# Kernel tuning notes

Hardware: AMD Instinct MI355X
Metric: run time of the kernel (lower is better)

Reference implementation:

```python
import jax, jax.numpy as jnp
import numpy as np

B, S, D, H = 2, 2048, 1024, 16
DK = D // H


def setup_inputs() -> dict:
    key = jax.random.key(0)
    ks = jax.random.split(key, 12)
    scale = 1.0 / np.sqrt(D)
    inp = {
        "q": jax.random.normal(ks[0], (B, S, D), jnp.float32),
        "k": jax.random.normal(ks[1], (B, S, D), jnp.float32),
        "v": jax.random.normal(ks[2], (B, S, D), jnp.float32),
        # causal mask: 1 = attend, 0 = mask, broadcastable to (B, 1, S, S)
        "mask": jnp.tril(jnp.ones((S, S), jnp.int32))[None, None, :, :],
        "Wq": jax.random.normal(ks[3], (D, D), jnp.float32) * scale,
        "bq": jax.random.normal(ks[4], (D,), jnp.float32) * scale,
        "Wk": jax.random.normal(ks[5], (D, D), jnp.float32) * scale,
        "bk": jax.random.normal(ks[6], (D,), jnp.float32) * scale,
        "Wv": jax.random.normal(ks[7], (D, D), jnp.float32) * scale,
        "bv": jax.random.normal(ks[8], (D,), jnp.float32) * scale,
        "Wo": jax.random.normal(ks[9], (D, D), jnp.float32) * scale,
        "bo": jax.random.normal(ks[10], (D,), jnp.float32) * scale,
    }
    return inp


def _split_heads(x):
    b, s, _ = x.shape
    return x.reshape(b, s, H, DK).transpose(0, 2, 1, 3)  # (b, h, s, dk)


def reference(q, k, v, mask, Wq, bq, Wk, bk, Wv, bv, Wo, bo):
    Q = _split_heads(q @ Wq.T + bq)
    K = _split_heads(k @ Wk.T + bk)
    V = _split_heads(v @ Wv.T + bv)
    scores = jnp.einsum("bhqd,bhkd->bhqk", Q, K) * (DK ** -0.5)
    scores = jnp.where(mask == 0, -jnp.inf, scores)
    attn = jax.nn.softmax(scores, axis=-1)  # dropout p=0.0 -> identity
    out = jnp.einsum("bhqk,bhkd->bhqd", attn, V)
    out = out.transpose(0, 2, 1, 3).reshape(q.shape[0], q.shape[1], D)
    return out @ Wo.T + bo
```

## Files before the change

### kernel.cpp

```cpp
#include <hip/hip_runtime.h>


#define S_LEN 2048
#define NHEAD 16
#define DMODEL 1024
#define DKH 64
#define LDA 72

typedef unsigned short u16;
typedef __attribute__((ext_vector_type(4))) short short4v;
typedef __attribute__((ext_vector_type(8))) short short8;
typedef __attribute__((ext_vector_type(8))) __bf16 bf16x8;
typedef __attribute__((ext_vector_type(4))) float f32x4;

__device__ inline u16 f2bf(float f) {
  return __builtin_bit_cast(u16, (__bf16)f);
}

__device__ inline f32x4 mfma16x16(bf16x8 a, bf16x8 b, f32x4 c) {
  return __builtin_amdgcn_mfma_f32_16x16x32_bf16(a, b, c, 0, 0, 0);
}

__device__ inline short8 pack8(float4 a, float4 b) {
  short8 r;
  r[0] = (short)f2bf(a.x); r[1] = (short)f2bf(a.y);
  r[2] = (short)f2bf(a.z); r[3] = (short)f2bf(a.w);
  r[4] = (short)f2bf(b.x); r[5] = (short)f2bf(b.y);
  r[6] = (short)f2bf(b.z); r[7] = (short)f2bf(b.w);
  return r;
}

typedef const __attribute__((address_space(1))) unsigned GU32;
typedef __attribute__((address_space(3))) unsigned LU32;
__device__ inline void gl2lds16(const void* g, void* l) {
  __builtin_amdgcn_global_load_lds((GU32*)g, (LU32*)l, 16, 0, 0);
}

#define SWZ(row, col8) (((row) * 8 + ((col8) ^ ((row) & 7))) * 8)

__global__ __launch_bounds__(256)
void conv_bf16(const float* __restrict__ w0, const float* __restrict__ w1,
               const float* __restrict__ w2, const float* __restrict__ w3,
               const float* __restrict__ aq, const float* __restrict__ ak,
               const float* __restrict__ av,
               u16* __restrict__ o0, u16* __restrict__ o1,
               u16* __restrict__ o2, u16* __restrict__ o3,
               u16* __restrict__ oq, u16* __restrict__ ok, u16* __restrict__ ov)
{
  const int y = blockIdx.y;
  const float* s; u16* d; int n;
  switch (y) {
    case 0: s = w0; d = o0; n = 1 << 20; break;
    case 1: s = w1; d = o1; n = 1 << 20; break;
    case 2: s = w2; d = o2; n = 1 << 20; break;
    case 3: s = w3; d = o3; n = 1 << 20; break;
    case 4: s = aq; d = oq; n = 1 << 22; break;
    case 5: s = ak; d = ok; n = 1 << 22; break;
    default: s = av; d = ov; n = 1 << 22; break;
  }
  const int i = (blockIdx.x * 256 + threadIdx.x) * 8;
  if (i >= n) return;
  float4 a = *(const float4*)&s[i];
  float4 b = *(const float4*)&s[i + 4];
  *(short8*)&d[i] = pack8(a, b);
}

__global__ __launch_bounds__(256)
void conv_w(const float* __restrict__ w0, const float* __restrict__ w1,
            const float* __restrict__ w2, const float* __restrict__ w3,
            u16* __restrict__ o0, u16* __restrict__ o1,
            u16* __restrict__ o2, u16* __restrict__ o3)
{
  const int z = blockIdx.y;
  const float* s = z == 0 ? w0 : z == 1 ? w1 : z == 2 ? w2 : w3;
  u16* d = z == 0 ? o0 : z == 1 ? o1 : z == 2 ? o2 : o3;
  const int i = (blockIdx.x * 256 + threadIdx.x) * 8;
  float4 a = *(const float4*)&s[i];
  float4 b = *(const float4*)&s[i + 4];
  *(short8*)&d[i] = pack8(a, b);
}

__global__ __launch_bounds__(256)
void proj_gemm_bf16(const u16* __restrict__ Aqb, const u16* __restrict__ Akb,
                    const u16* __restrict__ Avb,
                    const u16* __restrict__ Bq, const u16* __restrict__ Bk,
                    const u16* __restrict__ Bv,
                    const float* __restrict__ cq, const float* __restrict__ ck,
                    const float* __restrict__ cv,
                    u16* __restrict__ Oq, u16* __restrict__ Ok, u16* __restrict__ Ov)
{
  __shared__ u16 SM[4 * 8192];

  const int hw = blockIdx.x + (blockIdx.y << 3) + (blockIdx.z << 8);
  const int xcd = hw & 7, sq = hw >> 3;
  const int pan = sq % 12, xb = sq / 12;
  const int p = pan * 8 + xcd;
  const int zz = p >> 5, py = p & 31;

  const u16* Ab = zz == 0 ? Aqb : zz == 1 ? Akb : Avb;
  const u16* Wb = zz == 0 ? Bq : zz == 1 ? Bk : Bv;
  const float* bias = zz == 0 ? cq : zz == 1 ? ck : cv;

  const int t = threadIdx.x;
  const int lane = t & 63;
  const int wv = t >> 6;
  const int wm = wv >> 1, wn = wv & 1;
  const int g = lane >> 4, lr = lane & 15;
  const int bm = py << 7, bn = xb << 7;
  const int K = DMODEL;

  auto STAGE = [&](int buf, int kt) {
    const int k0 = kt << 6;
    u16* Asb = SM + buf * 8192;
    u16* Bsb = SM + 16384 + buf * 8192;
#pragma unroll
    for (int i = 0; i < 4; ++i) {
      int c = t + (i << 8);
      int row = c >> 3, col8 = c & 7;
      int c8s = col8 ^ (row & 7);
      gl2lds16(&Ab[(size_t)(bm + row) * K + k0 + c8s * 8], &Asb[c * 8]);
      gl2lds16(&Wb[(size_t)(bn + row) * K + k0 + c8s * 8], &Bsb[c * 8]);
    }
  };

  f32x4 acc[4][4] = {};
  STAGE(0, 0);
  __syncthreads();
  for (int kt = 0; kt < 16; ++kt) {
    const int cur = kt & 1;
    if (kt + 1 < 16) STAGE(cur ^ 1, kt + 1);
    u16* Asb = SM + cur * 8192;
    u16* Bsb = SM + 16384 + cur * 8192;
    bf16x8 af[2][4], bf[2][4];
#pragma unroll
    for (int kc = 0; kc < 2; ++kc)
#pragma unroll
      for (int f = 0; f < 4; ++f) {
        af[kc][f] = *(const bf16x8*)&Asb[SWZ(wm * 64 + f * 16 + lr, kc * 4 + g)];
        bf[kc][f] = *(const bf16x8*)&Bsb[SWZ(wn * 64 + f * 16 + lr, kc * 4 + g)];
      }
#pragma unroll
    for (int kc = 0; kc < 2; ++kc)
#pragma unroll
      for (int fm = 0; fm < 4; ++fm)
#pragma unroll
        for (int fn = 0; fn < 4; ++fn)
          acc[fm][fn] = mfma16x16(af[kc][fm], bf[kc][fn], acc[fm][fn]);
    __syncthreads();
  }

  if (zz == 2) {
    u16* TL = SM;
    const int b = bm >> 11, s0 = bm & (S_LEN - 1), h0 = bn >> 6;
#pragma unroll
    for (int hh = 0; hh < 2; ++hh) {
      __syncthreads();
      if (wn == hh) {
#pragma unroll
        for (int fm = 0; fm < 4; ++fm)
#pragma unroll
          for (int fn = 0; fn < 4; ++fn) {
            const int lch = fn * 16 + lr;
            const float bb = bias[bn + hh * 64 + lch];
#pragma unroll
            for (int r = 0; r < 4; ++r)
              TL[lch * 132 + wm * 64 + fm * 16 + g * 4 + r] = f2bf(acc[fm][fn][r] + bb);
          }
      }
      __syncthreads();
#pragma unroll
      for (int i = 0; i < 4; ++i) {
        int c = t + (i << 8);
        int dk = c >> 4, sc = (c & 15) << 3;
        short8 vv = *(const short8*)&TL[dk * 132 + sc];
        *(short8*)&Ov[(((size_t)(b * NHEAD + h0 + hh)) * DKH + dk) * S_LEN + s0 + sc] = vv;
      }
    }
  } else {
    u16* Out = zz == 0 ? Oq : Ok;
#pragma unroll
    for (int fm = 0; fm < 4; ++fm)
#pragma unroll
      for (int fn = 0; fn < 4; ++fn) {
        const int col = bn + wn * 64 + fn * 16 + lr;
        const int h = col >> 6, dk = col & (DKH - 1);
        const float bb = bias[col];
#pragma unroll
        for (int r = 0; r < 4; ++r) {
          const int row = bm + wm * 64 + fm * 16 + g * 4 + r;
          const int b = row >> 11, s = row & (S_LEN - 1);
          Out[(((size_t)(b * NHEAD + h)) * S_LEN + s) * DKH + dk] = f2bf(acc[fm][fn][r] + bb);
        }
      }
  }
}

__global__ __launch_bounds__(256)
void proj_gemm_f32(const float* __restrict__ Aq, const float* __restrict__ Akk,
                   const float* __restrict__ Av,
                   const u16* __restrict__ Bq, const u16* __restrict__ Bk,
                   const u16* __restrict__ Bv,
                   const float* __restrict__ cq, const float* __restrict__ ck,
                   const float* __restrict__ cv,
                   u16* __restrict__ Oq, u16* __restrict__ Ok, u16* __restrict__ Ov)
{
  __shared__ u16 SM[3 * 8192];
  u16* As = SM;
  u16* Bs0 = SM + 8192;
  u16* Bs1 = SM + 16384;

  const int hw = blockIdx.x + (blockIdx.y << 3) + (blockIdx.z << 8);
  const int xcd = hw & 7, sq = hw >> 3;
  const int pan = sq % 12, xb = sq / 12;
  const int p = pan * 8 + xcd;
  const int zz = p >> 5, py = p & 31;

  const float* Af = zz == 0 ? Aq : zz == 1 ? Akk : Av;
  const u16* Wb = zz == 0 ? Bq : zz == 1 ? Bk : Bv;
  const float* bias = zz == 0 ? cq : zz == 1 ? ck : cv;

  const int t = threadIdx.x;
  const int lane = t & 63;
  const int wv = t >> 6;
  const int wm = wv >> 1, wn = wv & 1;
  const int g = lane >> 4, lr = lane & 15;
  const int bm = py << 7, bn = xb << 7;
  const int K = DMODEL;

  float4 ax[4], ay[4];
  auto ALOAD = [&](int kt) {
    const int k0 = kt << 6;
#pragma unroll
    for (int i = 0; i < 4; ++i) {
      int c = t + (i << 8);
      int row = c >> 3, col8 = c & 7;
      const float* src = &Af[(size_t)(bm + row) * K + k0 + col8 * 8];
      ax[i] = *(const float4*)src;
      ay[i] = *(const float4*)(src + 4);
    }
  };
  auto AWRITE = [&]() {
#pragma unroll
    for (int i = 0; i < 4; ++i) {
      int c = t + (i << 8);
      int row = c >> 3, col8 = c & 7;
      *(short8*)&As[SWZ(row, col8)] = pack8(ax[i], ay[i]);
    }
  };
  auto BSTAGE = [&](u16* buf, int kt) {
    const int k0 = kt << 6;
#pragma unroll
    for (int i = 0; i < 4; ++i) {
      int c = t + (i << 8);
      int row = c >> 3, col8 = c & 7;
      int c8s = col8 ^ (row & 7);
      gl2lds16(&Wb[(size_t)(bn + row) * K + k0 + c8s * 8], &buf[c * 8]);
    }
  };

  f32x4 acc[4][4] = {};
  ALOAD(0);
  BSTAGE(Bs0, 0);
  AWRITE();
  __syncthreads();
  for (int kt = 0; kt < 16; ++kt) {
    u16* Bcur = (kt & 1) ? Bs1 : Bs0;
    u16* Bnxt = (kt & 1) ? Bs0 : Bs1;
    const bool more = (kt + 1 < 16);
    if (more) { ALOAD(kt + 1); BSTAGE(Bnxt, kt + 1); }
    bf16x8 af[2][4], bf[2][4];
#pragma unroll
    for (int kc = 0; kc < 2; ++kc)
#pragma unroll
      for (int f = 0; f < 4; ++f) {
        af[kc][f] = *(const bf16x8*)&As[SWZ(wm * 64 + f * 16 + lr, kc * 4 + g)];
        bf[kc][f] = *(const bf16x8*)&Bcur[SWZ(wn * 64 + f * 16 + lr, kc * 4 + g)];
      }
#pragma unroll
    for (int kc = 0; kc < 2; ++kc)
#pragma unroll
      for (int fm = 0; fm < 4; ++fm)
#pragma unroll
        for (int fn = 0; fn < 4; ++fn)
          acc[fm][fn] = mfma16x16(af[kc][fm], bf[kc][fn], acc[fm][fn]);
    __syncthreads();
    if (more) {
      AWRITE();
      __syncthreads();
    }
  }

  if (zz == 2) {
    u16* TL = SM;
    const int b = bm >> 11, s0 = bm & (S_LEN - 1), h0 = bn >> 6;
#pragma unroll
    for (int hh = 0; hh < 2; ++hh) {
      __syncthreads();
      if (wn == hh) {
#pragma unroll
        for (int fm = 0; fm < 4; ++fm)
#pragma unroll
          for (int fn = 0; fn < 4; ++fn) {
            const int lch = fn * 16 + lr;
            const float bb = bias[bn + hh * 64 + lch];
#pragma unroll
            for (int r = 0; r < 4; ++r)
              TL[lch * 132 + wm * 64 + fm * 16 + g * 4 + r] = f2bf(acc[fm][fn][r] + bb);
          }
      }
      __syncthreads();
#pragma unroll
      for (int i = 0; i < 4; ++i) {
        int c = t + (i << 8);
        int dk = c >> 4, sc = (c & 15) << 3;
        short8 vv = *(const short8*)&TL[dk * 132 + sc];
        *(short8*)&Ov[(((size_t)(b * NHEAD + h0 + hh)) * DKH + dk) * S_LEN + s0 + sc] = vv;
      }
    }
  } else {
    u16* Out = zz == 0 ? Oq : Ok;
#pragma unroll
    for (int fm = 0; fm < 4; ++fm)
#pragma unroll
      for (int fn = 0; fn < 4; ++fn) {
        const int col = bn + wn * 64 + fn * 16 + lr;
        const int h = col >> 6, dk = col & (DKH - 1);
        const float bb = bias[col];
#pragma unroll
        for (int r = 0; r < 4; ++r) {
          const int row = bm + wm * 64 + fm * 16 + g * 4 + r;
          const int b = row >> 11, s = row & (S_LEN - 1);
          Out[(((size_t)(b * NHEAD + h)) * S_LEN + s) * DKH + dk] = f2bf(acc[fm][fn][r] + bb);
        }
      }
  }
}

__global__ __launch_bounds__(256)
void out_gemm(const u16* __restrict__ Ao, const u16* __restrict__ Wb,
              const float* __restrict__ bias, float* __restrict__ Out)
{
  __shared__ u16 SM[4 * 8192];
  const int hw = blockIdx.x + (blockIdx.y << 3);
  const int xcd = hw & 7, sq = hw >> 3;
  const int pan = sq & 3, xb = sq >> 2;
  const int prow = pan * 8 + xcd;

  const int t = threadIdx.x;
  const int lane = t & 63;
  const int wv = t >> 6;
  const int wm = wv >> 1, wn = wv & 1;
  const int g = lane >> 4, lr = lane & 15;
  const int bm = prow << 7, bn = xb << 7;
  const int K = DMODEL;

  auto STAGE = [&](int buf, int kt) {
    const int k0 = kt << 6;
    u16* Asb = SM + buf * 8192;
    u16* Bsb = SM + 16384 + buf * 8192;
#pragma unroll
    for (int i = 0; i < 4; ++i) {
      int c = t + (i << 8);
      int row = c >> 3, col8 = c & 7;
      int c8s = col8 ^ (row & 7);
      int grow = bm + row;
      int b = grow >> 11, s = grow & (S_LEN - 1);
      int k = k0 + c8s * 8;
      int h = k >> 6, dk = k & (DKH - 1);
      gl2lds16(&Ao[(((size_t)(b * NHEAD + h)) * S_LEN + s) * DKH + dk], &Asb[c * 8]);
      gl2lds16(&Wb[(size_t)(bn + row) * K + k0 + c8s * 8], &Bsb[c * 8]);
    }
  };

  f32x4 acc[4][4] = {};
  STAGE(0, 0);
  __syncthreads();
  for (int kt = 0; kt < 16; ++kt) {
    const int cur = kt & 1;
    if (kt + 1 < 16) STAGE(cur ^ 1, kt + 1);
    u16* Asb = SM + cur * 8192;
    u16* Bsb = SM + 16384 + cur * 8192;
    bf16x8 af[2][4], bf[2][4];
#pragma unroll
    for (int kc = 0; kc < 2; ++kc)
#pragma unroll
      for (int f = 0; f < 4; ++f) {
        af[kc][f] = *(const bf16x8*)&Asb[SWZ(wm * 64 + f * 16 + lr, kc * 4 + g)];
        bf[kc][f] = *(const bf16x8*)&Bsb[SWZ(wn * 64 + f * 16 + lr, kc * 4 + g)];
      }
#pragma unroll
    for (int kc = 0; kc < 2; ++kc)
#pragma unroll
      for (int fm = 0; fm < 4; ++fm)
#pragma unroll
        for (int fn = 0; fn < 4; ++fn)
          acc[fm][fn] = mfma16x16(af[kc][fm], bf[kc][fn], acc[fm][fn]);
    __syncthreads();
  }
#pragma unroll
  for (int fm = 0; fm < 4; ++fm)
#pragma unroll
    for (int fn = 0; fn < 4; ++fn) {
      const int col = bn + wn * 64 + fn * 16 + lr;
      const float bb = bias[col];
#pragma unroll
      for (int r = 0; r < 4; ++r) {
        const int row = bm + wm * 64 + fm * 16 + g * 4 + r;
        Out[(size_t)row * DMODEL + col] = acc[fm][fn][r] + bb;
      }
    }
}

__global__ __launch_bounds__(256)
void attn_fwd(const u16* __restrict__ Qh, const u16* __restrict__ Kh,
              const u16* __restrict__ Vtg, u16* __restrict__ Ao)
{
  __shared__ u16 Ks[2][64 * LDA];
  __shared__ u16 Vs[2][64 * LDA];
  __shared__ u16 Ps[4][16 * LDA];
  const int t = threadIdx.x, lane = t & 63, w = t >> 6;
  const int g = lane >> 4, lr = lane & 15;
  const int bh = blockIdx.y;
  const int pA = blockIdx.x;
  const int tA = pA, tB = 31 - pA;
  const u16* Qb = Qh + (size_t)bh * S_LEN * DKH;
  const u16* Kb = Kh + (size_t)bh * S_LEN * DKH;
  const u16* Vb = Vtg + (size_t)bh * DKH * S_LEN;

  bf16x8 qfA[2], qfB[2];
#pragma unroll
  for (int kc = 0; kc < 2; ++kc) {
    qfA[kc] = *(const bf16x8*)&Qb[(size_t)(tA * 64 + w * 16 + lr) * DKH + kc * 32 + g * 8];
    qfB[kc] = *(const bf16x8*)&Qb[(size_t)(tB * 64 + w * 16 + lr) * DKH + kc * 32 + g * 8];
  }

  f32x4 oA[4] = {}, oB[4] = {};
  float mA = -1e30f, lA = 0.f, mB = -1e30f, lB = 0.f;

  const int r0 = t >> 3;
  const int c0 = (t & 7) << 3;
  short8 kr0, kr1, vr0, vr1;

  auto LOADT = [&](int kt) {
    const int kv0 = kt << 6;
    kr0 = *(const short8*)&Kb[(size_t)(kv0 + r0) * DKH + c0];
    kr1 = *(const short8*)&Kb[(size_t)(kv0 + r0 + 32) * DKH + c0];
    vr0 = *(const short8*)&Vb[(size_t)r0 * S_LEN + kv0 + c0];
    vr1 = *(const short8*)&Vb[(size_t)(r0 + 32) * S_LEN + kv0 + c0];
  };
  auto WRITET = [&](int b) {
    *(short8*)&Ks[b][r0 * LDA + c0] = kr0;
    *(short8*)&Ks[b][(r0 + 32) * LDA + c0] = kr1;
    *(short8*)&Vs[b][r0 * LDA + c0] = vr0;
    *(short8*)&Vs[b][(r0 + 32) * LDA + c0] = vr1;
  };

  auto COMPUTE = [&](int buf, const bf16x8* qf, f32x4* o, float& m, float& l,
                     bool diag) {
    f32x4 sf[4];
#pragma unroll
    for (int fk = 0; fk < 4; ++fk) {
      f32x4 a = {};
#pragma unroll
      for (int kc = 0; kc < 2; ++kc) {
        bf16x8 kf = *(const bf16x8*)&Ks[buf][(fk * 16 + lr) * LDA + kc * 32 + g * 8];
        a = mfma16x16(kf, qf[kc], a);
      }
      sf[fk] = a;
    }
    if (diag) {
#pragma unroll
      for (int fk = 0; fk < 4; ++fk)
#pragma unroll
        for (int r = 0; r < 4; ++r)
          if (fk * 16 + 4 * g + r > w * 16 + lr) sf[fk][r] = -1e30f;
    }
    float pm = fmaxf(fmaxf(sf[0][0], sf[0][1]), fmaxf(sf[0][2], sf[0][3]));
#pragma unroll
    for (int fk = 1; fk < 4; ++fk)
      pm = fmaxf(pm, fmaxf(fmaxf(sf[fk][0], sf[fk][1]), fmaxf(sf[fk][2], sf[fk][3])));
    pm = fmaxf(pm, __shfl_xor(pm, 16, 64));
    pm = fmaxf(pm, __shfl_xor(pm, 32, 64));
    float alpha = 1.0f;
    if (!__all(pm - m <= 64.0f)) {
      float mn = fmaxf(m, pm);
      alpha = __expf((m - mn) * 0.125f);
      m = mn;
#pragma unroll
      for (int r = 0; r < 4; ++r) {
        float ar = __shfl(alpha, 4 * g + r, 64);
#pragma unroll
        for (int d = 0; d < 4; ++d) o[d][r] *= ar;
      }
    }
    float rs = 0.f;
#pragma unroll
    for (int fk = 0; fk < 4; ++fk) {
      float p0 = __expf((sf[fk][0] - m) * 0.125f);
      float p1 = __expf((sf[fk][1] - m) * 0.125f);
      float p2 = __expf((sf[fk][2] - m) * 0.125f);
      float p3 = __expf((sf[fk][3] - m) * 0.125f);
      rs += (p0 + p1) + (p2 + p3);
      short4v pk;
      pk[0] = (short)f2bf(p0); pk[1] = (short)f2bf(p1);
      pk[2] = (short)f2bf(p2); pk[3] = (short)f2bf(p3);
      *(short4v*)&Ps[w][lr * LDA + fk * 16 + 4 * g] = pk;
    }
    rs += __shfl_xor(rs, 16, 64);
    rs += __shfl_xor(rs, 32, 64);
    l = l * alpha + rs;
#pragma unroll
    for (int kc = 0; kc < 2; ++kc) {
      bf16x8 pf = *(const bf16x8*)&Ps[w][lr * LDA + kc * 32 + g * 8];
#pragma unroll
      for (int df = 0; df < 4; ++df) {
        bf16x8 vf = *(const bf16x8*)&Vs[buf][(df * 16 + lr) * LDA + kc * 32 + g * 8];
        o[df] = mfma16x16(pf, vf, o[df]);
      }
    }
  };

  const int nt = tB + 1;
  LOADT(0);
  WRITET(0);
  for (int kt = 0; kt < nt; ++kt) {
    const int cur = kt & 1;
    const bool more = (kt + 1 < nt);
    if (more) LOADT(kt + 1);
    __syncthreads();
    if (kt <= tA) COMPUTE(cur, qfA, oA, mA, lA, kt == tA);
    COMPUTE(cur, qfB, oB, mB, lB, kt == tB);
    if (more) WRITET(cur ^ 1);
  }

  float iA[4], iB[4];
#pragma unroll
  for (int r = 0; r < 4; ++r) {
    iA[r] = __builtin_amdgcn_rcpf(__shfl(lA, 4 * g + r, 64));
    iB[r] = __builtin_amdgcn_rcpf(__shfl(lB, 4 * g + r, 64));
  }
#pragma unroll
  for (int df = 0; df < 4; ++df)
#pragma unroll
    for (int r = 0; r < 4; ++r) {
      const int d = df * 16 + lr;
      const int qa = tA * 64 + w * 16 + g * 4 + r;
      const int qb2 = tB * 64 + w * 16 + g * 4 + r;
      Ao[((size_t)bh * S_LEN + qa) * DKH + d] = f2bf(oA[df][r] * iA[r]);
      Ao[((size_t)bh * S_LEN + qb2) * DKH + d] = f2bf(oB[df][r] * iB[r]);
    }
}

extern "C" void kernel_launch(void* const* d_in, const int* in_sizes, int n_in,
                              void* d_out, int out_size, void* d_ws, size_t ws_size,
                              hipStream_t stream)
{
  (void)in_sizes; (void)n_in; (void)out_size;
  const float* q  = (const float*)d_in[0];
  const float* k  = (const float*)d_in[1];
  const float* v  = (const float*)d_in[2];
  const float* Wq = (const float*)d_in[4];
  const float* bq = (const float*)d_in[5];
  const float* Wk = (const float*)d_in[6];
  const float* bk = (const float*)d_in[7];
  const float* Wv = (const float*)d_in[8];
  const float* bv = (const float*)d_in[9];
  const float* Wo = (const float*)d_in[10];
  const float* bo = (const float*)d_in[11];

  char* ws = (char*)d_ws;
  const size_t MB = 1024 * 1024;

  if (ws_size >= 56 * MB) {
    u16* Wqb = (u16*)(ws);
    u16* Wkb = (u16*)(ws + 2 * MB);
    u16* Wvb = (u16*)(ws + 4 * MB);
    u16* Wob = (u16*)(ws + 6 * MB);
    u16* qb  = (u16*)(ws + 8 * MB);
    u16* kb  = (u16*)(ws + 16 * MB);
    u16* vb  = (u16*)(ws + 24 * MB);
    u16* Qh  = (u16*)(ws + 32 * MB);
    u16* Kh  = (u16*)(ws + 40 * MB);
    u16* Vt  = (u16*)(ws + 48 * MB);
    u16* Ao  = qb;

    conv_bf16<<<dim3(2048, 7), 256, 0, stream>>>(Wq, Wk, Wv, Wo, q, k, v,
                                                 Wqb, Wkb, Wvb, Wob, qb, kb, vb);
    proj_gemm_bf16<<<dim3(8, 32, 3), 256, 0, stream>>>(qb, kb, vb, Wqb, Wkb, Wvb,
                                                       bq, bk, bv, Qh, Kh, Vt);
    attn_fwd<<<dim3(16, 2 * NHEAD), 256, 0, stream>>>(Qh, Kh, Vt, Ao);
    out_gemm<<<dim3(8, 32), 256, 0, stream>>>(Ao, Wob, bo, (float*)d_out);
  } else {
    u16* Wqb = (u16*)(ws);
    u16* Wkb = (u16*)(ws + 2 * MB);
    u16* Wvb = (u16*)(ws + 4 * MB);
    u16* Wob = (u16*)(ws + 6 * MB);
    u16* Qh  = (u16*)(ws + 8 * MB);
    u16* Kh  = (u16*)(ws + 16 * MB);
    u16* Vt  = (u16*)(ws + 24 * MB);
    u16* Ao  = (u16*)(ws + 32 * MB);

    conv_w<<<dim3(512, 4), 256, 0, stream>>>(Wq, Wk, Wv, Wo, Wqb, Wkb, Wvb, Wob);
    proj_gemm_f32<<<dim3(8, 32, 3), 256, 0, stream>>>(q, k, v, Wqb, Wkb, Wvb,
                                                      bq, bk, bv, Qh, Kh, Vt);
    attn_fwd<<<dim3(16, 2 * NHEAD), 256, 0, stream>>>(Qh, Kh, Vt, Ao);
    out_gemm<<<dim3(8, 32), 256, 0, stream>>>(Ao, Wob, bo, (float*)d_out);
  }
}
```

Measured before the change: 120.7 us.

## Split attention KV loop across two blocks and merge partial results

The attention kernel gains a split mode where each (pair-tile, head) is processed by two blocks that take alternating KV tiles, each writing a partially normalized output plus its row max and sum. A new merge kernel combines the two halves with softmax rescaling before the output projection. This doubles the attention grid from 512 blocks to improve occupancy across the CUs, at the cost of an extra kernel launch, extra global traffic for the partials, and a second bf16 rounding step. The fp32-input projection fallback is removed and the small-workspace path now reuses the bf16 conversion route.

```diff
diff --git a/kernel.cpp b/kernel.cpp
--- a/kernel.cpp
+++ b/kernel.cpp
@@ -15,6 +15,9 @@
 
 __device__ inline u16 f2bf(float f) {
   return __builtin_bit_cast(u16, (__bf16)f);
+}
+__device__ inline float bf2f(u16 x) {
+  return __builtin_bit_cast(float, ((unsigned)x) << 16);
 }
 
 __device__ inline f32x4 mfma16x16(bf16x8 a, bf16x8 b, f32x4 c) {
@@ -196,147 +199,6 @@
 }
 
 __global__ __launch_bounds__(256)
-void proj_gemm_f32(const float* __restrict__ Aq, const float* __restrict__ Akk,
-                   const float* __restrict__ Av,
-                   const u16* __restrict__ Bq, const u16* __restrict__ Bk,
-                   const u16* __restrict__ Bv,
-                   const float* __restrict__ cq, const float* __restrict__ ck,
-                   const float* __restrict__ cv,
-                   u16* __restrict__ Oq, u16* __restrict__ Ok, u16* __restrict__ Ov)
-{
-  __shared__ u16 SM[3 * 8192];
-  u16* As = SM;
-  u16* Bs0 = SM + 8192;
-  u16* Bs1 = SM + 16384;
-
-  const int hw = blockIdx.x + (blockIdx.y << 3) + (blockIdx.z << 8);
-  const int xcd = hw & 7, sq = hw >> 3;
-  const int pan = sq % 12, xb = sq / 12;
-  const int p = pan * 8 + xcd;
-  const int zz = p >> 5, py = p & 31;
-
-  const float* Af = zz == 0 ? Aq : zz == 1 ? Akk : Av;
-  const u16* Wb = zz == 0 ? Bq : zz == 1 ? Bk : Bv;
-  const float* bias = zz == 0 ? cq : zz == 1 ? ck : cv;
-
-  const int t = threadIdx.x;
-  const int lane = t & 63;
-  const int wv = t >> 6;
-  const int wm = wv >> 1, wn = wv & 1;
-  const int g = lane >> 4, lr = lane & 15;
-  const int bm = py << 7, bn = xb << 7;
-  const int K = DMODEL;
-
-  float4 ax[4], ay[4];
-  auto ALOAD = [&](int kt) {
-    const int k0 = kt << 6;
-#pragma unroll
-    for (int i = 0; i < 4; ++i) {
-      int c = t + (i << 8);
-      int row = c >> 3, col8 = c & 7;
-      const float* src = &Af[(size_t)(bm + row) * K + k0 + col8 * 8];
-      ax[i] = *(const float4*)src;
-      ay[i] = *(const float4*)(src + 4);
-    }
-  };
-  auto AWRITE = [&]() {
-#pragma unroll
-    for (int i = 0; i < 4; ++i) {
-      int c = t + (i << 8);
-      int row = c >> 3, col8 = c & 7;
-      *(short8*)&As[SWZ(row, col8)] = pack8(ax[i], ay[i]);
-    }
-  };
-  auto BSTAGE = [&](u16* buf, int kt) {
-    const int k0 = kt << 6;
-#pragma unroll
-    for (int i = 0; i < 4; ++i) {
-      int c = t + (i << 8);
-      int row = c >> 3, col8 = c & 7;
-      int c8s = col8 ^ (row & 7);
-      gl2lds16(&Wb[(size_t)(bn + row) * K + k0 + c8s * 8], &buf[c * 8]);
-    }
-  };
-
-  f32x4 acc[4][4] = {};
-  ALOAD(0);
-  BSTAGE(Bs0, 0);
-  AWRITE();
-  __syncthreads();
-  for (int kt = 0; kt < 16; ++kt) {
-    u16* Bcur = (kt & 1) ? Bs1 : Bs0;
-    u16* Bnxt = (kt & 1) ? Bs0 : Bs1;
-    const bool more = (kt + 1 < 16);
-    if (more) { ALOAD(kt + 1); BSTAGE(Bnxt, kt + 1); }
-    bf16x8 af[2][4], bf[2][4];
-#pragma unroll
-    for (int kc = 0; kc < 2; ++kc)
-#pragma unroll
-      for (int f = 0; f < 4; ++f) {
-        af[kc][f] = *(const bf16x8*)&As[SWZ(wm * 64 + f * 16 + lr, kc * 4 + g)];
-        bf[kc][f] = *(const bf16x8*)&Bcur[SWZ(wn * 64 + f * 16 + lr, kc * 4 + g)];
-      }
-#pragma unroll
-    for (int kc = 0; kc < 2; ++kc)
-#pragma unroll
-      for (int fm = 0; fm < 4; ++fm)
-#pragma unroll
-        for (int fn = 0; fn < 4; ++fn)
-          acc[fm][fn] = mfma16x16(af[kc][fm], bf[kc][fn], acc[fm][fn]);
-    __syncthreads();
-    if (more) {
-      AWRITE();
-      __syncthreads();
-    }
-  }
-
-  if (zz == 2) {
-    u16* TL = SM;
-    const int b = bm >> 11, s0 = bm & (S_LEN - 1), h0 = bn >> 6;
-#pragma unroll
-    for (int hh = 0; hh < 2; ++hh) {
-      __syncthreads();
-      if (wn == hh) {
-#pragma unroll
-        for (int fm = 0; fm < 4; ++fm)
-#pragma unroll
-          for (int fn = 0; fn < 4; ++fn) {
-            const int lch = fn * 16 + lr;
-            const float bb = bias[bn + hh * 64 + lch];
-#pragma unroll
-            for (int r = 0; r < 4; ++r)
-              TL[lch * 132 + wm * 64 + fm * 16 + g * 4 + r] = f2bf(acc[fm][fn][r] + bb);
-          }
-      }
-      __syncthreads();
-#pragma unroll
-      for (int i = 0; i < 4; ++i) {
-        int c = t + (i << 8);
-        int dk = c >> 4, sc = (c & 15) << 3;
-        short8 vv = *(const short8*)&TL[dk * 132 + sc];
-        *(short8*)&Ov[(((size_t)(b * NHEAD + h0 + hh)) * DKH + dk) * S_LEN + s0 + sc] = vv;
-      }
-    }
-  } else {
-    u16* Out = zz == 0 ? Oq : Ok;
-#pragma unroll
-    for (int fm = 0; fm < 4; ++fm)
-#pragma unroll
-      for (int fn = 0; fn < 4; ++fn) {
-        const int col = bn + wn * 64 + fn * 16 + lr;
-        const int h = col >> 6, dk = col & (DKH - 1);
-        const float bb = bias[col];
-#pragma unroll
-        for (int r = 0; r < 4; ++r) {
-          const int row = bm + wm * 64 + fm * 16 + g * 4 + r;
-          const int b = row >> 11, s = row & (S_LEN - 1);
-          Out[(((size_t)(b * NHEAD + h)) * S_LEN + s) * DKH + dk] = f2bf(acc[fm][fn][r] + bb);
-        }
-      }
-  }
-}
-
-__global__ __launch_bounds__(256)
 void out_gemm(const u16* __restrict__ Ao, const u16* __restrict__ Wb,
               const float* __restrict__ bias, float* __restrict__ Out)
 {
@@ -411,9 +273,11 @@
     }
 }
 
+template<bool SP>
 __global__ __launch_bounds__(256)
 void attn_fwd(const u16* __restrict__ Qh, const u16* __restrict__ Kh,
-              const u16* __restrict__ Vtg, u16* __restrict__ Ao)
+              const u16* __restrict__ Vtg, u16* __restrict__ Po,
+              float* __restrict__ ML)
 {
   __shared__ u16 Ks[2][64 * LDA];
   __shared__ u16 Vs[2][64 * LDA];
@@ -422,6 +286,7 @@
   const int g = lane >> 4, lr = lane & 15;
   const int bh = blockIdx.y;
   const int pA = blockIdx.x;
+  const int hf = SP ? blockIdx.z : 0;
   const int tA = pA, tB = 31 - pA;
   const u16* Qb = Qh + (size_t)bh * S_LEN * DKH;
   const u16* Kb = Kh + (size_t)bh * S_LEN * DKH;
@@ -520,25 +385,36 @@
     }
   };
 
-  const int nt = tB + 1;
-  LOADT(0);
+  const int step = SP ? 2 : 1;
+  LOADT(hf);
   WRITET(0);
-  for (int kt = 0; kt < nt; ++kt) {
-    const int cur = kt & 1;
-    const bool more = (kt + 1 < nt);
-    if (more) LOADT(kt + 1);
+  for (int kt = hf; kt <= tB; kt += step) {
+    const int cur = SP ? ((kt >> 1) & 1) : (kt & 1);
+    const bool more = kt + step <= tB;
+    if (more) LOADT(kt + step);
     __syncthreads();
     if (kt <= tA) COMPUTE(cur, qfA, oA, mA, lA, kt == tA);
     COMPUTE(cur, qfB, oB, mB, lB, kt == tB);
     if (more) WRITET(cur ^ 1);
   }
 
+  if (SP && lane < 16) {
+    const size_t mb = ((size_t)(hf * 2 * NHEAD + bh)) * S_LEN;
+    const int qa = tA * 64 + w * 16 + lr;
+    const int qb2 = tB * 64 + w * 16 + lr;
+    ML[(mb + qa) * 2] = mA;  ML[(mb + qa) * 2 + 1] = lA;
+    ML[(mb + qb2) * 2] = mB; ML[(mb + qb2) * 2 + 1] = lB;
+  }
+
   float iA[4], iB[4];
 #pragma unroll
   for (int r = 0; r < 4; ++r) {
-    iA[r] = __builtin_amdgcn_rcpf(__shfl(lA, 4 * g + r, 64));
-    iB[r] = __builtin_amdgcn_rcpf(__shfl(lB, 4 * g + r, 64));
-  }
+    float la = __shfl(lA, 4 * g + r, 64);
+    float lb = __shfl(lB, 4 * g + r, 64);
+    iA[r] = la > 0.f ? __builtin_amdgcn_rcpf(la) : 0.f;
+    iB[r] = lb > 0.f ? __builtin_amdgcn_rcpf(lb) : 0.f;
+  }
+  u16* Pd = Po + (SP ? (size_t)hf * 2 * NHEAD * S_LEN * DKH : 0);
 #pragma unroll
   for (int df = 0; df < 4; ++df)
 #pragma unroll
@@ -546,9 +422,31 @@
       const int d = df * 16 + lr;
       const int qa = tA * 64 + w * 16 + g * 4 + r;
       const int qb2 = tB * 64 + w * 16 + g * 4 + r;
-      Ao[((size_t)bh * S_LEN + qa) * DKH + d] = f2bf(oA[df][r] * iA[r]);
-      Ao[((size_t)bh * S_LEN + qb2) * DKH + d] = f2bf(oB[df][r] * iB[r]);
-    }
+      Pd[((size_t)bh * S_LEN + qa) * DKH + d] = f2bf(oA[df][r] * iA[r]);
+      Pd[((size_t)bh * S_LEN + qb2) * DKH + d] = f2bf(oB[df][r] * iB[r]);
+    }
+}
+
+#define HALF_E ((size_t)2 * NHEAD * S_LEN * DKH)
+#define HALF_R (2 * NHEAD * S_LEN)
+__global__ __launch_bounds__(256)
+void attn_merge(u16* __restrict__ Po, const float* __restrict__ ML)
+{
+  const size_t e = ((size_t)blockIdx.x * 256 + threadIdx.x) * 8;
+  const size_t row = e >> 6;
+  const float m0 = ML[row * 2], l0 = ML[row * 2 + 1];
+  const float m1 = ML[(HALF_R + row) * 2], l1 = ML[(HALF_R + row) * 2 + 1];
+  const float mm = fmaxf(m0, m1);
+  const float w0 = l0 * __expf((m0 - mm) * 0.125f);
+  const float w1 = l1 * __expf((m1 - mm) * 0.125f);
+  const float inv = __builtin_amdgcn_rcpf(w0 + w1);
+  short8 a = *(const short8*)&Po[e];
+  short8 b = *(const short8*)&Po[HALF_E + e];
+  short8 o;
+#pragma unroll
+  for (int j = 0; j < 8; ++j)
+    o[j] = (short)f2bf((bf2f((u16)a[j]) * w0 + bf2f((u16)b[j]) * w1) * inv);
+  *(short8*)&Po[e] = o;
 }
 
 extern "C" void kernel_launch(void* const* d_in, const int* in_sizes, int n_in,
@@ -571,39 +469,30 @@
   char* ws = (char*)d_ws;
   const size_t MB = 1024 * 1024;
 
+  u16* Wqb = (u16*)(ws);
+  u16* Wkb = (u16*)(ws + 2 * MB);
+  u16* Wvb = (u16*)(ws + 4 * MB);
+  u16* Wob = (u16*)(ws + 6 * MB);
+  u16* qb  = (u16*)(ws + 8 * MB);
+  u16* kb  = (u16*)(ws + 16 * MB);
+  u16* vb  = (u16*)(ws + 24 * MB);
+  u16* Qh  = (u16*)(ws + 32 * MB);
+  u16* Kh  = (u16*)(ws + 40 * MB);
+  u16* Vt  = (u16*)(ws + 48 * MB);
+
+  conv_bf16<<<dim3(2048, 7), 256, 0, stream>>>(Wq, Wk, Wv, Wo, q, k, v,
+                                               Wqb, Wkb, Wvb, Wob, qb, kb, vb);
+  proj_gemm_bf16<<<dim3(8, 32, 3), 256, 0, stream>>>(qb, kb, vb, Wqb, Wkb, Wvb,
+                                                     bq, bk, bv, Qh, Kh, Vt);
   if (ws_size >= 56 * MB) {
-    u16* Wqb = (u16*)(ws);
-    u16* Wkb = (u16*)(ws + 2 * MB);
-    u16* Wvb = (u16*)(ws + 4 * MB);
-    u16* Wob = (u16*)(ws + 6 * MB);
-    u16* qb  = (u16*)(ws + 8 * MB);
-    u16* kb  = (u16*)(ws + 16 * MB);
-    u16* vb  = (u16*)(ws + 24 * MB);
-    u16* Qh  = (u16*)(ws + 32 * MB);
-    u16* Kh  = (u16*)(ws + 40 * MB);
-    u16* Vt  = (u16*)(ws + 48 * MB);
-    u16* Ao  = qb;
-
-    conv_bf16<<<dim3(2048, 7), 256, 0, stream>>>(Wq, Wk, Wv, Wo, q, k, v,
-                                                 Wqb, Wkb, Wvb, Wob, qb, kb, vb);
-    proj_gemm_bf16<<<dim3(8, 32, 3), 256, 0, stream>>>(qb, kb, vb, Wqb, Wkb, Wvb,
-                                                       bq, bk, bv, Qh, Kh, Vt);
-    attn_fwd<<<dim3(16, 2 * NHEAD), 256, 0, stream>>>(Qh, Kh, Vt, Ao);
+    u16* Po = qb;
+    float* ML = (float*)vb;
+    attn_fwd<true><<<dim3(16, 2 * NHEAD, 2), 256, 0, stream>>>(Qh, Kh, Vt, Po, ML);
+    attn_merge<<<dim3(2048), 256, 0, stream>>>(Po, ML);
+    out_gemm<<<dim3(8, 32), 256, 0, stream>>>(Po, Wob, bo, (float*)d_out);
+  } else {
+    u16* Ao = qb;
+    attn_fwd<false><<<dim3(16, 2 * NHEAD), 256, 0, stream>>>(Qh, Kh, Vt, Ao, nullptr);
     out_gemm<<<dim3(8, 32), 256, 0, stream>>>(Ao, Wob, bo, (float*)d_out);
-  } else {
-    u16* Wqb = (u16*)(ws);
-    u16* Wkb = (u16*)(ws + 2 * MB);
-    u16* Wvb = (u16*)(ws + 4 * MB);
-    u16* Wob = (u16*)(ws + 6 * MB);
-    u16* Qh  = (u16*)(ws + 8 * MB);
-    u16* Kh  = (u16*)(ws + 16 * MB);
-    u16* Vt  = (u16*)(ws + 24 * MB);
-    u16* Ao  = (u16*)(ws + 32 * MB);
-
-    conv_w<<<dim3(512, 4), 256, 0, stream>>>(Wq, Wk, Wv, Wo, Wqb, Wkb, Wvb, Wob);
-    proj_gemm_f32<<<dim3(8, 32, 3), 256, 0, stream>>>(q, k, v, Wqb, Wkb, Wvb,
-                                                      bq, bk, bv, Qh, Kh, Vt);
-    attn_fwd<<<dim3(16, 2 * NHEAD), 256, 0, stream>>>(Qh, Kh, Vt, Ao);
-    out_gemm<<<dim3(8, 32), 256, 0, stream>>>(Ao, Wob, bo, (float*)d_out);
-  }
-}
+  }
+}
```

After: 127.0 us. +5.2%, slower.
